# Optimization experiments

Hardware: AMD Instinct MI355X
Metric: run time of the kernel (lower is better)

## Reference

```python
import jax, jax.numpy as jnp
import numpy as np

B, T, FEAT, MD, PROJ, DEC = 32768, 50, 14, 3, 128, 128
DT = 0.1           # hard-coded integration step in original rollout
ALPHA = 0.3        # keras LeakyReLU default alpha
DUMMY_DX = 50.0    # dummy_value_set['em_delta_x']
DUMMY_DV = 0.0     # dummy_value_set['em_delta_v']


def setup_inputs() -> dict:
    key = jax.random.key(0)
    ks = jax.random.split(key, 12)
    d_in = PROJ + DEC + 8 + MD  # 267
    idm_s = jax.random.normal(ks[2], (B, T, FEAT), jnp.float32)
    # last feature is the m_veh_exists 0/1 flag
    idm_s = idm_s.at[:, :, -1].set((idm_s[:, :, -1] > 0).astype(jnp.float32))
    return {
        "proj_latent": jax.random.normal(ks[0], (B, PROJ), jnp.float32),
        "enc_h": jax.random.normal(ks[1], (B, DEC), jnp.float32),
        "idm_s": idm_s,
        "merger_cs": jax.random.normal(ks[3], (B, T, MD), jnp.float32),
        "env_mean": jax.random.normal(ks[4], (8,), jnp.float32),
        "env_var": jax.random.uniform(ks[5], (8,), jnp.float32) + 0.5,  # keep away from 0
        "W1": jax.random.normal(ks[6], (d_in, DEC), jnp.float32) * 0.05,
        "b1": jnp.zeros((DEC,), jnp.float32),
        "W2": jax.random.normal(ks[7], (DEC, DEC), jnp.float32) * 0.05,
        "b2": jnp.zeros((DEC,), jnp.float32),
        "W3": jax.random.normal(ks[8], (DEC, 1), jnp.float32) * 0.05,
        "b3": jnp.zeros((1,), jnp.float32),
    }


def _leaky(x):
    return jnp.where(x >= 0, x, ALPHA * x)


def reference(proj_latent, enc_h, idm_s, merger_cs, env_mean, env_var,
              W1, b1, W2, b2, W3, b3):
    inv_std = 1.0 / jnp.sqrt(env_var)  # scale_env_s uses var_**0.5

    def mlp(x):  # att_layer_1 -> att_layer_2 -> action_neu
        h = _leaky(x @ W1 + b1)
        h = _leaky(h @ W2 + b2)
        return h @ W3 + b3  # [B,1]

    # initial physics state from timestep 0
    ego_v0 = idm_s[:, 0, 0:1]    # [B,1]
    ego_a0 = idm_s[:, 0, 11:12]
    ego_x0 = idm_s[:, 0, 3:4]
    disp0 = jnp.zeros_like(ego_v0)

    def step(carry, xs):
        ego_v, ego_a, ego_x, disp = carry
        idm_t, mc_t = xs  # [B,FEAT], [B,MD]  (timestep step-1)
        f_veh_v = idm_t[:, 1:2]
        m_veh_v = idm_t[:, 2:3]
        f_glob_x = idm_t[:, 4:5]
        m_glob_x = idm_t[:, 5:6]
        f_veh_a = idm_t[:, 12:13]
        m_exists = idm_t[:, -1:]
        ef_dx = f_glob_x - ego_x
        em_dx = (m_glob_x - ego_x) * m_exists + (1.0 - m_exists) * DUMMY_DX
        ef_dv = ego_v - f_veh_v
        em_dv = (ego_v - m_veh_v) * m_exists + (1.0 - m_exists) * DUMMY_DV
        env = jnp.concatenate([ego_v, f_veh_v, ego_a, f_veh_a,
                               ef_dv, ef_dx, em_dv, em_dx], axis=-1)  # [B,8]
        env = (env - env_mean) * inv_std
        inp = jnp.concatenate([proj_latent, enc_h, env, mc_t], axis=-1)  # [B,267]
        a_new = mlp(inp)  # [B,1]
        move = ego_v * DT + 0.5 * a_new * DT * DT
        disp_new = disp + move
        ego_x_new = ego_x + move
        ego_v_new = ego_v + a_new * DT
        return (ego_v_new, a_new, ego_x_new, disp_new), (a_new, disp_new)

    xs = (jnp.swapaxes(idm_s, 0, 1), jnp.swapaxes(merger_cs, 0, 1))  # [T,B,*]
    _, (acts, disps) = jax.lax.scan(step, (ego_v0, ego_a0, ego_x0, disp0), xs)
    act_seq = jnp.swapaxes(acts, 0, 1)    # [B,T,1]
    disp_seq = jnp.swapaxes(disps, 0, 1)  # [B,T,1]
    displacement_seq = jnp.concatenate([disp0[:, None, :], disp_seq], axis=1)  # [B,T+1,1]
    return displacement_seq, act_seq
```

## Files before the change

kernel.cpp:

```cpp
#include <hip/hip_runtime.h>


using bf16x8 = __attribute__((ext_vector_type(8))) short;
using f32x16 = __attribute__((ext_vector_type(16))) float;

constexpr int B_TOT   = 32768;
constexpr int T_STEPS = 50;
constexpr int FEATC   = 14;
constexpr int MDC     = 3;
constexpr float ALPHA_C = 0.3f;
constexpr float DT_C    = 0.1f;

constexpr int NB   = 64;
constexpr int NTHR = 512;
constexpr int H1S  = 130;
constexpr int ENVS = 18;

__device__ __forceinline__ float leaky(float x) { return fmaxf(x, ALPHA_C * x); }

__device__ __forceinline__ short2 split1(float x) {
    unsigned u = __float_as_uint(x);
    short h = (short)(u >> 16);
    float r = x - __uint_as_float(u & 0xFFFF0000u);
    short l = (short)(__float_as_uint(r) >> 16);
    return make_short2(h, l);
}

#define MFMA(A, B, C) __builtin_amdgcn_mfma_f32_32x32x16_bf16(A, B, C, 0, 0, 0)

__launch_bounds__(NTHR, 2)
__global__ void fwd_sim(const float* __restrict__ proj,
                        const float* __restrict__ enc,
                        const float* __restrict__ idm,
                        const float* __restrict__ mc,
                        const float* __restrict__ env_mean,
                        const float* __restrict__ env_var,
                        const float* __restrict__ W1,
                        const float* __restrict__ b1,
                        const float* __restrict__ W2,
                        const float* __restrict__ b2,
                        const float* __restrict__ W3,
                        const float* __restrict__ b3,
                        float* __restrict__ out)
{
    __shared__ float s_h1[NB * H1S];
    __shared__ float s_env[NB * ENVS];

    const int tid  = threadIdx.x;
    const int lane = tid & 63;
    const int w    = tid >> 6;
    const int mh   = w >> 2;
    const int nq   = w & 3;
    const int l31  = lane & 31;
    const int half = lane >> 5;
    const int ncol = nq * 32 + l31;
    const int am   = mh * 32 + l31;
    const int b_base = blockIdx.x * NB;
    const long ACT_OFF = (long)B_TOT * 51;

    for (int i = tid; i < NB * ENVS; i += NTHR) s_env[i] = 0.f;
    __syncthreads();

    const float b1v = b1[ncol];
    const float b2v = b2[ncol];
    const float w3v = W3[ncol];

    bf16x8 w2h[8], w2l[8];
    for (int kb = 0; kb < 8; ++kb) {
        #pragma unroll
        for (int j = 0; j < 8; ++j) {
            short2 s = split1(W2[(kb * 16 + half * 8 + j) * 128 + ncol]);
            w2h[kb][j] = s.x; w2l[kb][j] = s.y;
        }
    }
    bf16x8 w1xh, w1xl;
    #pragma unroll
    for (int j = 0; j < 8; ++j) {
        int k = half * 8 + j;
        short2 s = split1(k < 11 ? W1[(256 + k) * 128 + ncol] : 0.f);
        w1xh[j] = s.x; w1xl[j] = s.y;
    }

    f32x16 base;
    #pragma unroll
    for (int r = 0; r < 16; ++r) base[r] = b1v;
    for (int kb = 0; kb < 16; ++kb) {
        const float* src = (kb < 8) ? proj : enc;
        const int kloc = (kb & 7) * 16 + half * 8;
        const float* ap = src + (long)(b_base + am) * 128 + kloc;
        float av[8];
        *(float4*)(av)     = *(const float4*)(ap);
        *(float4*)(av + 4) = *(const float4*)(ap + 4);
        bf16x8 ah, al, bh, bl;
        #pragma unroll
        for (int j = 0; j < 8; ++j) {
            short2 s = split1(av[j]);
            ah[j] = s.x; al[j] = s.y;
        }
        #pragma unroll
        for (int j = 0; j < 8; ++j) {
            short2 s = split1(W1[(kb * 16 + half * 8 + j) * 128 + ncol]);
            bh[j] = s.x; bl[j] = s.y;
        }
        base = MFMA(ah, bh, base);
        base = MFMA(al, bh, base);
        base = MFMA(ah, bl, base);
    }

    const bool act = (tid & 7) == 0;
    const int  sm  = tid >> 3;
    const long sb  = b_base + sm;
    float ego_v = 0.f, ego_a = 0.f, ego_x = 0.f, disp = 0.f, b3r = 0.f;
    float mn[8], is[8];
    float nv1 = 0.f, nv2 = 0.f, nv4 = 0.f, nv5 = 0.f, nv12 = 0.f, nv13 = 0.f;
    float nm0 = 0.f, nm1 = 0.f, nm2 = 0.f;
    if (act) {
        #pragma unroll
        for (int k = 0; k < 8; ++k) { mn[k] = env_mean[k]; is[k] = rsqrtf(env_var[k]); }
        b3r = b3[0];
        const float* r0 = idm + sb * (T_STEPS * FEATC);
        const float* m0 = mc  + sb * (T_STEPS * MDC);
        ego_v = r0[0]; ego_a = r0[11]; ego_x = r0[3]; disp = 0.f;
        out[sb * 51] = 0.f;
        float e[8];
        e[0] = ego_v; e[1] = r0[1]; e[2] = ego_a; e[3] = r0[12];
        e[4] = ego_v - r0[1];
        e[5] = r0[4] - ego_x;
        e[6] = (ego_v - r0[2]) * r0[13];
        e[7] = (r0[5] - ego_x) * r0[13] + (1.f - r0[13]) * 50.f;
        #pragma unroll
        for (int k = 0; k < 8; ++k) s_env[sm * ENVS + k] = (e[k] - mn[k]) * is[k];
        s_env[sm * ENVS + 8]  = m0[0];
        s_env[sm * ENVS + 9]  = m0[1];
        s_env[sm * ENVS + 10] = m0[2];
        nv1 = r0[FEATC + 1]; nv2 = r0[FEATC + 2]; nv4 = r0[FEATC + 4];
        nv5 = r0[FEATC + 5]; nv12 = r0[FEATC + 12]; nv13 = r0[FEATC + 13];
        nm0 = m0[MDC]; nm1 = m0[MDC + 1]; nm2 = m0[MDC + 2];
    }
    __syncthreads();

    for (int t = 0; t < T_STEPS; ++t) {
        {
            const float* ep = s_env + am * ENVS + half * 8;
            float av[8];
            *(float2*)(av)     = *(const float2*)(ep);
            *(float2*)(av + 2) = *(const float2*)(ep + 2);
            *(float2*)(av + 4) = *(const float2*)(ep + 4);
            *(float2*)(av + 6) = *(const float2*)(ep + 6);
            bf16x8 ah, al;
            #pragma unroll
            for (int j = 0; j < 8; ++j) {
                short2 s = split1(av[j]);
                ah[j] = s.x; al[j] = s.y;
            }
            f32x16 acc = base;
            acc = MFMA(ah, w1xh, acc);
            acc = MFMA(al, w1xh, acc);
            acc = MFMA(ah, w1xl, acc);
            #pragma unroll
            for (int r = 0; r < 16; ++r) {
                int row = (r & 3) + 8 * (r >> 2) + 4 * half + mh * 32;
                s_h1[row * H1S + ncol] = leaky(acc[r]);
            }
        }
        __syncthreads();

        bf16x8 ah2[8], al2[8];
        #pragma unroll
        for (int kb = 0; kb < 8; ++kb) {
            const float* hp = s_h1 + am * H1S + kb * 16 + half * 8;
            float av[8];
            *(float2*)(av)     = *(const float2*)(hp);
            *(float2*)(av + 2) = *(const float2*)(hp + 2);
            *(float2*)(av + 4) = *(const float2*)(hp + 4);
            *(float2*)(av + 6) = *(const float2*)(hp + 6);
            #pragma unroll
            for (int j = 0; j < 8; ++j) {
                short2 s = split1(av[j]);
                ah2[kb][j] = s.x; al2[kb][j] = s.y;
            }
        }
        __syncthreads();

        {
            f32x16 acc;
            #pragma unroll
            for (int r = 0; r < 16; ++r) acc[r] = b2v;
            #pragma unroll
            for (int kb = 0; kb < 8; ++kb) {
                acc = MFMA(ah2[kb], w2h[kb], acc);
                acc = MFMA(al2[kb], w2h[kb], acc);
                acc = MFMA(ah2[kb], w2l[kb], acc);
            }
            #pragma unroll
            for (int r = 0; r < 16; ++r) {
                int row = (r & 3) + 8 * (r >> 2) + 4 * half + mh * 32;
                s_h1[row * H1S + ncol] = leaky(acc[r]) * w3v;
            }
        }
        __syncthreads();

        {
            const int row = tid >> 3, seg = tid & 7;
            const float* pp = s_h1 + row * H1S + seg * 16;
            float s = 0.f;
            #pragma unroll
            for (int i = 0; i < 8; ++i) {
                float2 v = *(const float2*)(pp + i * 2);
                s += v.x + v.y;
            }
            s += __shfl_xor(s, 1);
            s += __shfl_xor(s, 2);
            s += __shfl_xor(s, 4);
            if (act) {
                const float a = s + b3r;
                const float move = ego_v * DT_C + 0.5f * a * DT_C * DT_C;
                disp  += move;
                ego_x += move;
                ego_v += a * DT_C;
                ego_a  = a;
                out[sb * 51 + t + 1] = disp;
                out[ACT_OFF + sb * 50 + t] = a;
                if (t < T_STEPS - 1) {
                    float e[8];
                    e[0] = ego_v; e[1] = nv1; e[2] = ego_a; e[3] = nv12;
                    e[4] = ego_v - nv1;
                    e[5] = nv4 - ego_x;
                    e[6] = (ego_v - nv2) * nv13;
                    e[7] = (nv5 - ego_x) * nv13 + (1.f - nv13) * 50.f;
                    #pragma unroll
                    for (int k = 0; k < 8; ++k) s_env[sm * ENVS + k] = (e[k] - mn[k]) * is[k];
                    s_env[sm * ENVS + 8]  = nm0;
                    s_env[sm * ENVS + 9]  = nm1;
                    s_env[sm * ENVS + 10] = nm2;
                    const int tn = (t + 2 < T_STEPS) ? t + 2 : T_STEPS - 1;
                    const float* rn = idm + sb * (T_STEPS * FEATC) + tn * FEATC;
                    const float* mrn = mc + sb * (T_STEPS * MDC) + tn * MDC;
                    nv1 = rn[1]; nv2 = rn[2]; nv4 = rn[4]; nv5 = rn[5];
                    nv12 = rn[12]; nv13 = rn[13];
                    nm0 = mrn[0]; nm1 = mrn[1]; nm2 = mrn[2];
                }
            }
        }
        __syncthreads();
    }
}

extern "C" void kernel_launch(void* const* d_in, const int* in_sizes, int n_in,
                              void* d_out, int out_size, void* d_ws, size_t ws_size,
                              hipStream_t stream) {
    const float* proj     = (const float*)d_in[0];
    const float* enc      = (const float*)d_in[1];
    const float* idm      = (const float*)d_in[2];
    const float* mcs      = (const float*)d_in[3];
    const float* env_mean = (const float*)d_in[4];
    const float* env_var  = (const float*)d_in[5];
    const float* W1       = (const float*)d_in[6];
    const float* b1       = (const float*)d_in[7];
    const float* W2       = (const float*)d_in[8];
    const float* b2       = (const float*)d_in[9];
    const float* W3       = (const float*)d_in[10];
    const float* b3       = (const float*)d_in[11];

    fwd_sim<<<B_TOT / NB, NTHR, 0, stream>>>(
        proj, enc, idm, mcs, env_mean, env_var,
        W1, b1, W2, b2, W3, b3, (float*)d_out);
}
```

Measured before the change: 445.9 us.

## Store layer-1 activations pre-split as packed bf16 hi/lo and drop a barrier

Layer-1 outputs are now split into bf16 high/low halves once at write time and stored packed in one 32-bit word, so the layer-2 reader only does 128-bit LDS loads plus byte permutes instead of float loads and per-element splitting. A separate shared buffer for the layer-2 partial products lets the barrier between reading h1 and overwriting it be removed. The row stride changes to 132 to allow aligned vector loads. In exchange LDS use grows, which may affect the two-blocks-per-CU occupancy, and the padding change may alter bank conflicts.

Result: faster. 401.8 us (-9.9%).

```diff
diff --git a/kernel.cpp b/kernel.cpp
--- a/kernel.cpp
+++ b/kernel.cpp
@@ -3,6 +3,7 @@
 
 using bf16x8 = __attribute__((ext_vector_type(8))) short;
 using f32x16 = __attribute__((ext_vector_type(16))) float;
+using u32x4  = __attribute__((ext_vector_type(4))) unsigned int;
 
 constexpr int B_TOT   = 32768;
 constexpr int T_STEPS = 50;
@@ -13,7 +14,7 @@
 
 constexpr int NB   = 64;
 constexpr int NTHR = 512;
-constexpr int H1S  = 130;
+constexpr int PS   = 132;
 constexpr int ENVS = 18;
 
 __device__ __forceinline__ float leaky(float x) { return fmaxf(x, ALPHA_C * x); }
@@ -24,6 +25,12 @@
     float r = x - __uint_as_float(u & 0xFFFF0000u);
     short l = (short)(__float_as_uint(r) >> 16);
     return make_short2(h, l);
+}
+
+__device__ __forceinline__ unsigned packsplit(float x) {
+    unsigned u = __float_as_uint(x);
+    float r = x - __uint_as_float(u & 0xFFFF0000u);
+    return (u >> 16) | (__float_as_uint(r) & 0xFFFF0000u);
 }
 
 #define MFMA(A, B, C) __builtin_amdgcn_mfma_f32_32x32x16_bf16(A, B, C, 0, 0, 0)
@@ -43,8 +50,9 @@
                         const float* __restrict__ b3,
                         float* __restrict__ out)
 {
-    __shared__ float s_h1[NB * H1S];
-    __shared__ float s_env[NB * ENVS];
+    __shared__ unsigned s_h1p[NB * PS];
+    __shared__ float    s_p  [NB * PS];
+    __shared__ float    s_env[NB * ENVS];
 
     const int tid  = threadIdx.x;
     const int lane = tid & 63;
@@ -64,6 +72,10 @@
     const float b1v = b1[ncol];
     const float b2v = b2[ncol];
     const float w3v = W3[ncol];
+
+    unsigned*       wp = s_h1p + (mh * 32 + 4 * half) * PS + ncol;
+    const unsigned* rp = s_h1p + am * PS + half * 8;
+    float*          pw = s_p   + (mh * 32 + 4 * half) * PS + ncol;
 
     bf16x8 w2h[8], w2l[8];
     for (int kb = 0; kb < 8; ++kb) {
@@ -159,25 +171,8 @@
             acc = MFMA(ah, w1xl, acc);
             #pragma unroll
             for (int r = 0; r < 16; ++r) {
-                int row = (r & 3) + 8 * (r >> 2) + 4 * half + mh * 32;
-                s_h1[row * H1S + ncol] = leaky(acc[r]);
-            }
-        }
-        __syncthreads();
-
-        bf16x8 ah2[8], al2[8];
-        #pragma unroll
-        for (int kb = 0; kb < 8; ++kb) {
-            const float* hp = s_h1 + am * H1S + kb * 16 + half * 8;
-            float av[8];
-            *(float2*)(av)     = *(const float2*)(hp);
-            *(float2*)(av + 2) = *(const float2*)(hp + 2);
-            *(float2*)(av + 4) = *(const float2*)(hp + 4);
-            *(float2*)(av + 6) = *(const float2*)(hp + 6);
-            #pragma unroll
-            for (int j = 0; j < 8; ++j) {
-                short2 s = split1(av[j]);
-                ah2[kb][j] = s.x; al2[kb][j] = s.y;
+                const int roff = (r & 3) + 8 * (r >> 2);
+                wp[roff * PS] = packsplit(leaky(acc[r]));
             }
         }
         __syncthreads();
@@ -188,21 +183,34 @@
             for (int r = 0; r < 16; ++r) acc[r] = b2v;
             #pragma unroll
             for (int kb = 0; kb < 8; ++kb) {
-                acc = MFMA(ah2[kb], w2h[kb], acc);
-                acc = MFMA(al2[kb], w2h[kb], acc);
-                acc = MFMA(ah2[kb], w2l[kb], acc);
+                u32x4 q0 = *reinterpret_cast<const u32x4*>(rp + kb * 16);
+                u32x4 q1 = *reinterpret_cast<const u32x4*>(rp + kb * 16 + 4);
+                u32x4 hh, ll;
+                hh[0] = __builtin_amdgcn_perm(q0[1], q0[0], 0x05040100u);
+                hh[1] = __builtin_amdgcn_perm(q0[3], q0[2], 0x05040100u);
+                hh[2] = __builtin_amdgcn_perm(q1[1], q1[0], 0x05040100u);
+                hh[3] = __builtin_amdgcn_perm(q1[3], q1[2], 0x05040100u);
+                ll[0] = __builtin_amdgcn_perm(q0[1], q0[0], 0x07060302u);
+                ll[1] = __builtin_amdgcn_perm(q0[3], q0[2], 0x07060302u);
+                ll[2] = __builtin_amdgcn_perm(q1[1], q1[0], 0x07060302u);
+                ll[3] = __builtin_amdgcn_perm(q1[3], q1[2], 0x07060302u);
+                bf16x8 ah2 = __builtin_bit_cast(bf16x8, hh);
+                bf16x8 al2 = __builtin_bit_cast(bf16x8, ll);
+                acc = MFMA(ah2, w2h[kb], acc);
+                acc = MFMA(al2, w2h[kb], acc);
+                acc = MFMA(ah2, w2l[kb], acc);
             }
             #pragma unroll
             for (int r = 0; r < 16; ++r) {
-                int row = (r & 3) + 8 * (r >> 2) + 4 * half + mh * 32;
-                s_h1[row * H1S + ncol] = leaky(acc[r]) * w3v;
+                const int roff = (r & 3) + 8 * (r >> 2);
+                pw[roff * PS] = leaky(acc[r]) * w3v;
             }
         }
         __syncthreads();
 
         {
             const int row = tid >> 3, seg = tid & 7;
-            const float* pp = s_h1 + row * H1S + seg * 16;
+            const float* pp = s_p + row * PS + seg * 16;
             float s = 0.f;
             #pragma unroll
             for (int i = 0; i < 8; ++i) {
```
